# Kernel tuning notes

Measured on AMD Instinct MI355X. Metric: run time of the kernel, lower is better.

The kernel has to match this reference:

```python
import jax, jax.numpy as jnp
import numpy as np

LB_WEIGHT = 0.01  # load_balance_loss_weight


def setup_inputs() -> dict:
    key = jax.random.key(0)
    ks = jax.random.split(key, 5)
    B, S, D, F, E = 2, 2048, 1024, 4096, 8
    scale = 0.02
    return {
        "x": jax.random.normal(ks[0], (B, S, D), dtype=jnp.float32),
        "Wr": jax.random.normal(ks[1], (E, D), dtype=jnp.float32) * scale,
        "W1": jax.random.normal(ks[2], (E, F, D), dtype=jnp.float32) * scale,
        "b1": jnp.zeros((E, F), dtype=jnp.float32),
        "W2": jax.random.normal(ks[3], (E, D, F), dtype=jnp.float32) * scale,
        "b2": jnp.zeros((E, D), dtype=jnp.float32),
        "top_k": 2,
    }


def reference(x, Wr, W1, b1, W2, b2, top_k):
    B, S, D = x.shape
    E = Wr.shape[0]
    x_flat = x.reshape(-1, D)                      # (T, D)

    # Router: softmax over experts, then top-k with renormalized gates.
    router_logits = x_flat @ Wr.T                  # (T, E)
    router_probs = jax.nn.softmax(router_logits, axis=-1)
    topk_p, topk_idx = jax.lax.top_k(router_probs, top_k)   # (T, K)
    topk_p = topk_p / jnp.sum(topk_p, axis=-1, keepdims=True)

    # Combine weights per expert: w[t, e] = sum_k topk_p[t, k] * [idx[t, k] == e]
    one_hot = jax.nn.one_hot(topk_idx, E, dtype=x.dtype)     # (T, K, E)
    combine = jnp.einsum("tk,tke->te", topk_p, one_hot)      # (T, E)

    # Expert FFNs (dense over all experts; masked-out experts get zero weight).
    # FeedForward: Linear(D->F) -> GELU -> Linear(F->D); dropout is identity (eval).
    h = jnp.einsum("td,efd->tef", x_flat, W1) + b1           # (T, E, F)
    h = jax.nn.gelu(h)
    expert_out = jnp.einsum("tef,edf->ted", h, W2) + b2      # (T, E, D)

    out_flat = jnp.einsum("te,ted->td", combine, expert_out) # (T, D)
    output = out_flat.reshape(B, S, D)

    # Load-balance aux loss.
    expert_usage = jnp.mean(router_probs, axis=0)            # (E,)
    aux_loss = LB_WEIGHT * jnp.sum((expert_usage - 1.0 / E) ** 2)
    return output, aux_loss
```

## Files before the change

kernel.cpp:

```cpp
#include <hip/hip_runtime.h>
#include <hip/hip_bf16.h>
#include <stdint.h>

#define D_DIM 1024
#define F_DIM 4096
#define E_NUM 8
#define BM2 256
#define BN2 256
#define BK 64
#define MAXTILES 80
#define MAXT256 40

typedef __attribute__((ext_vector_type(4))) float f32x4;
typedef __attribute__((ext_vector_type(8))) short bf16x8;

#define C_CNT   0
#define C_CUR   8
#define C_OFF   16
#define C_NT    25
#define C_TE    26
#define C_TR    (26+MAXTILES)
#define C_USAGE (26+2*MAXTILES)

__device__ __forceinline__ void gload_lds16(const void* g, void* l) {
  __builtin_amdgcn_global_load_lds((const __attribute__((address_space(1))) void*)g,
                                   (__attribute__((address_space(3))) void*)l, 16, 0, 0);
}

__device__ __forceinline__ float bf2f(unsigned short u) {
  union { unsigned int i; float f; } c; c.i = ((unsigned int)u) << 16; return c.f;
}

__global__ void cvt_k(const float* __restrict__ s, unsigned short* __restrict__ d, int n4) {
  const int stride = gridDim.x * blockDim.x;
  for (int i = blockIdx.x * blockDim.x + threadIdx.x; i < n4; i += stride) {
    float4 v = ((const float4*)s)[i];
    __hip_bfloat16 h0 = __float2bfloat16(v.x);
    __hip_bfloat16 h1 = __float2bfloat16(v.y);
    __hip_bfloat16 h2 = __float2bfloat16(v.z);
    __hip_bfloat16 h3 = __float2bfloat16(v.w);
    ushort4 o;
    o.x = *(unsigned short*)&h0; o.y = *(unsigned short*)&h1;
    o.z = *(unsigned short*)&h2; o.w = *(unsigned short*)&h3;
    ((ushort4*)d)[i] = o;
  }
}

__global__ __launch_bounds__(256) void router_k(
    const float* __restrict__ x, const float* __restrict__ Wr,
    int* __restrict__ t2i, float* __restrict__ t2g,
    float* __restrict__ usage_part, unsigned short* __restrict__ xb, int T) {
  __shared__ float us[4][E_NUM];
  const int wave = threadIdx.x >> 6;
  const int lane = threadIdx.x & 63;
  const int gw = blockIdx.x * 4 + wave;
  const float4* xt = (const float4*)(x + (size_t)gw * D_DIM);
  const float4* wr4 = (const float4*)Wr;
  unsigned short* xrow = xb + (size_t)gw * D_DIM;
  float l[E_NUM] = {0.f,0.f,0.f,0.f,0.f,0.f,0.f,0.f};
#pragma unroll
  for (int it = 0; it < D_DIM / 256; it++) {
    const int i4 = it * 64 + lane;
    const float4 xv = xt[i4];
    __hip_bfloat16 c0 = __float2bfloat16(xv.x), c1 = __float2bfloat16(xv.y);
    __hip_bfloat16 c2 = __float2bfloat16(xv.z), c3 = __float2bfloat16(xv.w);
    ushort4 ov; ov.x = *(unsigned short*)&c0; ov.y = *(unsigned short*)&c1;
    ov.z = *(unsigned short*)&c2; ov.w = *(unsigned short*)&c3;
    ((ushort4*)xrow)[i4] = ov;
#pragma unroll
    for (int e = 0; e < E_NUM; e++) {
      const float4 w = wr4[e * (D_DIM / 4) + i4];
      l[e] += xv.x * w.x + xv.y * w.y + xv.z * w.z + xv.w * w.w;
    }
  }
#pragma unroll
  for (int e = 0; e < E_NUM; e++) {
    float v = l[e];
    v += __shfl_xor(v, 32); v += __shfl_xor(v, 16); v += __shfl_xor(v, 8);
    v += __shfl_xor(v, 4);  v += __shfl_xor(v, 2);  v += __shfl_xor(v, 1);
    l[e] = v;
  }
  float m = l[0];
#pragma unroll
  for (int e = 1; e < E_NUM; e++) m = fmaxf(m, l[e]);
  float p[E_NUM]; float s = 0.f;
#pragma unroll
  for (int e = 0; e < E_NUM; e++) { p[e] = expf(l[e] - m); s += p[e]; }
  const float inv = 1.0f / s;
  float v1 = l[0]; int i1 = 0;
#pragma unroll
  for (int e = 1; e < E_NUM; e++) { if (l[e] > v1) { v1 = l[e]; i1 = e; } }
  float v2 = -3.0e38f; int i2 = 0;
#pragma unroll
  for (int e = 0; e < E_NUM; e++) { if (e != i1 && l[e] > v2) { v2 = l[e]; i2 = e; } }
  const float p1 = expf(v1 - m);
  const float p2 = expf(v2 - m);
  const float gd = 1.0f / (p1 + p2);
  if (lane == 0) {
    t2i[gw * 2] = i1; t2i[gw * 2 + 1] = i2;
    t2g[gw * 2] = p1 * gd; t2g[gw * 2 + 1] = p2 * gd;
#pragma unroll
    for (int e = 0; e < E_NUM; e++) us[wave][e] = p[e] * inv;
  }
  __syncthreads();
  if (threadIdx.x < E_NUM) {
    const int e = threadIdx.x;
    usage_part[blockIdx.x * E_NUM + e] = us[0][e] + us[1][e] + us[2][e] + us[3][e];
  }
}

__global__ __launch_bounds__(256) void reduce_k(
    const float* __restrict__ usage_part, const int* __restrict__ t2i,
    int* __restrict__ ctrl, int nblk, int T2) {
  __shared__ float usum[E_NUM];
  __shared__ int hist[E_NUM];
  if (threadIdx.x < E_NUM) { usum[threadIdx.x] = 0.f; hist[threadIdx.x] = 0; }
  __syncthreads();
  {
    const int e = threadIdx.x & 7;
    const int chunk = threadIdx.x >> 3;
    float s = 0.f;
    for (int i = chunk; i < nblk; i += 32) s += usage_part[i * E_NUM + e];
    atomicAdd(&usum[e], s);
  }
  {
    int h[E_NUM] = {0,0,0,0,0,0,0,0};
    for (int i = threadIdx.x; i < T2; i += 256) h[t2i[i] & 7]++;
#pragma unroll
    for (int e = 0; e < E_NUM; e++) if (h[e]) atomicAdd(&hist[e], h[e]);
  }
  __syncthreads();
  if (threadIdx.x < E_NUM) {
    ctrl[C_CNT + threadIdx.x] = hist[threadIdx.x];
    ((float*)(ctrl + C_USAGE))[threadIdx.x] = usum[threadIdx.x];
  }
}

__global__ void offsets_k(int* __restrict__ ctrl, float* __restrict__ aux_out, int T) {
  if (threadIdx.x == 0) {
    int off = 0, nt = 0;
    for (int e = 0; e < E_NUM; e++) {
      ctrl[C_OFF + e] = off;
      ctrl[C_CUR + e] = off;
      const int c = ctrl[C_CNT + e];
      const int ntile = (c + BM2 - 1) / BM2;
      for (int i = 0; i < ntile; i++) {
        ctrl[C_TE + nt] = e;
        ctrl[C_TR + nt] = off + i * BM2;
        nt++;
      }
      off += c;
    }
    ctrl[C_OFF + E_NUM] = off;
    ctrl[C_NT] = nt;
    const float* usage = (const float*)(ctrl + C_USAGE);
    float loss = 0.f;
    for (int e = 0; e < E_NUM; e++) {
      const float um = usage[e] / (float)T - 1.0f / (float)E_NUM;
      loss += um * um;
    }
    aux_out[0] = 0.01f * loss;
  }
}

__global__ void scatter_k(const int* __restrict__ t2i, int* __restrict__ ctrl,
                          int* __restrict__ rmap, int* __restrict__ slots, int T) {
  const int t = blockIdx.x * blockDim.x + threadIdx.x;
  if (t >= T) return;
#pragma unroll
  for (int k = 0; k < 2; k++) {
    const int e = t2i[t * 2 + k];
    const int slot = atomicAdd(&ctrl[C_CUR + e], 1);
    rmap[slot] = t;
    slots[t * 2 + k] = slot;
  }
}

#define STAGE(K0, AL, BL)                                            \
  {                                                                  \
    _Pragma("unroll")                                                \
    for (int i = 0; i < 4; i++) gload_lds16(a_src[i] + (K0), AL[i]); \
    _Pragma("unroll")                                                \
    for (int i = 0; i < 4; i++) gload_lds16(b_src[i] + (K0), BL[i]); \
  }

#define COMPUTE(AC, BC)                                              \
  {                                                                  \
    _Pragma("unroll")                                                \
    for (int kh = 0; kh < 2; ++kh) {                                 \
      const int co = (((kh * 4 + ckq) ^ swz) << 4);                  \
      bf16x8 af[8], bfv[4];                                          \
      _Pragma("unroll")                                              \
      for (int mi = 0; mi < 8; mi++)                                 \
        af[mi] = *(const bf16x8*)((AC) + (rA + mi * 16) * 128 + co); \
      _Pragma("unroll")                                              \
      for (int ni = 0; ni < 4; ni++)                                 \
        bfv[ni] = *(const bf16x8*)((BC) + (rB + ni * 16) * 128 + co);\
      _Pragma("unroll")                                              \
      for (int mi = 0; mi < 8; mi++)                                 \
        _Pragma("unroll")                                            \
        for (int ni = 0; ni < 4; ni++)                               \
          acc[mi][ni] = __builtin_amdgcn_mfma_f32_16x16x32_bf16(af[mi], bfv[ni], acc[mi][ni], 0, 0, 0); \
    }                                                                \
  }

__global__ __launch_bounds__(512, 2) void gemm1_k(
    const unsigned short* __restrict__ xb, const unsigned short* __restrict__ W1b,
    const float* __restrict__ b1, unsigned short* __restrict__ hb,
    const int* __restrict__ rmap, const int* __restrict__ ctrl, int T2) {
  extern __shared__ char smem[];
  const int lin = blockIdx.x;
  const int lin2 = (lin & 7) * 80 + (lin >> 3);
  const int tile = lin2 >> 4;
  const int fbase = (lin2 & 15) * BN2;

  const int nt = ctrl[C_NT];
  if (tile >= nt) return;
  const int e = ctrl[C_TE + tile];
  const int rowbase = ctrl[C_TR + tile];
  const int row_end = ctrl[C_OFF + e + 1];

  const int tid = threadIdx.x;
  const int lane = tid & 63;
  const int wave = tid >> 6;

  const unsigned short* a_src[4];
  const unsigned short* b_src[4];
  char *aL0[4], *bL0[4], *aL1[4], *bL1[4];
#pragma unroll
  for (int i = 0; i < 4; i++) {
    const int c = tid + 512 * i;
    const int r = c >> 3, cc = c & 7;
    const int sc = cc ^ (r & 7);
    int pos = rowbase + r; pos = pos < T2 ? pos : T2 - 1;
    a_src[i] = xb + (size_t)rmap[pos] * D_DIM + sc * 8;
    b_src[i] = W1b + ((size_t)e * F_DIM + (size_t)(fbase + r)) * D_DIM + sc * 8;
    const int dst = wave * 1024 + i * 8192;
    aL0[i] = smem + dst;          aL1[i] = smem + 32768 + dst;
    bL0[i] = smem + 65536 + dst;  bL1[i] = smem + 98304 + dst;
  }
  const char* As0 = smem;          const char* As1 = smem + 32768;
  const char* Bs0 = smem + 65536;  const char* Bs1 = smem + 98304;

  f32x4 acc[8][4] = {};
  const int wm = wave >> 2, wn = wave & 3;
  const int rA = wm * 128 + (lane & 15);
  const int rB = wn * 64 + (lane & 15);
  const int swz = lane & 7;
  const int ckq = lane >> 4;

  STAGE(0, aL0, bL0);
  const int NK = D_DIM / BK;
  for (int kt = 0; kt < NK; kt += 2) {
    STAGE((kt + 1) * BK, aL1, bL1);
    asm volatile("s_waitcnt vmcnt(8)" ::: "memory");
    __builtin_amdgcn_s_barrier();
    __builtin_amdgcn_sched_barrier(0);
    COMPUTE(As0, Bs0);
    __builtin_amdgcn_sched_barrier(0);
    __builtin_amdgcn_s_barrier();
    if (kt + 2 < NK) {
      STAGE((kt + 2) * BK, aL0, bL0);
      asm volatile("s_waitcnt vmcnt(8)" ::: "memory");
    } else {
      asm volatile("s_waitcnt vmcnt(0)" ::: "memory");
    }
    __builtin_amdgcn_s_barrier();
    __builtin_amdgcn_sched_barrier(0);
    COMPUTE(As1, Bs1);
    __builtin_amdgcn_sched_barrier(0);
    __builtin_amdgcn_s_barrier();
  }

  const int r_rem = row_end - rowbase;
  const float* b1e = b1 + (size_t)e * F_DIM;
  float bias[4];
#pragma unroll
  for (int ni = 0; ni < 4; ni++)
    bias[ni] = b1e[fbase + wn * 64 + ni * 16 + (lane & 15)];
#pragma unroll
  for (int mi = 0; mi < 8; mi++) {
#pragma unroll
    for (int q = 0; q < 4; q++) {
      const int rr = wm * 128 + mi * 16 + (lane >> 4) * 4 + q;
      if (rr < r_rem) {
        unsigned short* hrow = hb + (size_t)(rowbase + rr) * F_DIM;
#pragma unroll
        for (int ni = 0; ni < 4; ni++) {
          const int col = fbase + wn * 64 + ni * 16 + (lane & 15);
          const float v = acc[mi][ni][q] + bias[ni];
          const float u2 = 1.5957691216057308f * (v + 0.044715f * v * v * v);
          const float gg = v / (1.0f + __expf(-u2));
          __hip_bfloat16 hv = __float2bfloat16(gg);
          hrow[col] = *(unsigned short*)&hv;
        }
      }
    }
  }
}

__global__ __launch_bounds__(512, 2) void gemm2_k(
    const unsigned short* __restrict__ hb, const unsigned short* __restrict__ W2b,
    unsigned short* __restrict__ y2, const int* __restrict__ ctrl, int T2) {
  extern __shared__ char smem[];
  const int lin = blockIdx.x;
  const int lin2 = (lin & 7) * 80 + (lin >> 3);
  const int tile = lin2 >> 4;
  const int rest = lin2 & 15;
  const int z = rest >> 2;
  const int dbase = (rest & 3) * BN2;

  const int nt = ctrl[C_NT];
  if (tile >= nt) return;
  const int e = ctrl[C_TE + tile];
  const int rowbase = ctrl[C_TR + tile];
  const int row_end = ctrl[C_OFF + e + 1];
  const int kt0 = z * (F_DIM / BK / 4);

  const int tid = threadIdx.x;
  const int lane = tid & 63;
  const int wave = tid >> 6;

  const unsigned short* a_src[4];
  const unsigned short* b_src[4];
  char *aL0[4], *bL0[4], *aL1[4], *bL1[4];
#pragma unroll
  for (int i = 0; i < 4; i++) {
    const int c = tid + 512 * i;
    const int r = c >> 3, cc = c & 7;
    const int sc = cc ^ (r & 7);
    int pos = rowbase + r; pos = pos < T2 ? pos : T2 - 1;
    a_src[i] = hb + (size_t)pos * F_DIM + sc * 8;
    b_src[i] = W2b + ((size_t)e * D_DIM + (size_t)(dbase + r)) * F_DIM + sc * 8;
    const int dst = wave * 1024 + i * 8192;
    aL0[i] = smem + dst;          aL1[i] = smem + 32768 + dst;
    bL0[i] = smem + 65536 + dst;  bL1[i] = smem + 98304 + dst;
  }
  const char* As0 = smem;          const char* As1 = smem + 32768;
  const char* Bs0 = smem + 65536;  const char* Bs1 = smem + 98304;

  f32x4 acc[8][4] = {};
  const int wm = wave >> 2, wn = wave & 3;
  const int rA = wm * 128 + (lane & 15);
  const int rB = wn * 64 + (lane & 15);
  const int swz = lane & 7;
  const int ckq = lane >> 4;

  const int NKH = F_DIM / BK / 4;
  STAGE(kt0 * BK, aL0, bL0);
  for (int kt = kt0; kt < kt0 + NKH; kt += 2) {
    STAGE((kt + 1) * BK, aL1, bL1);
    asm volatile("s_waitcnt vmcnt(8)" ::: "memory");
    __builtin_amdgcn_s_barrier();
    __builtin_amdgcn_sched_barrier(0);
    COMPUTE(As0, Bs0);
    __builtin_amdgcn_sched_barrier(0);
    __builtin_amdgcn_s_barrier();
    if (kt + 2 < kt0 + NKH) {
      STAGE((kt + 2) * BK, aL0, bL0);
      asm volatile("s_waitcnt vmcnt(8)" ::: "memory");
    } else {
      asm volatile("s_waitcnt vmcnt(0)" ::: "memory");
    }
    __builtin_amdgcn_s_barrier();
    __builtin_amdgcn_sched_barrier(0);
    COMPUTE(As1, Bs1);
    __builtin_amdgcn_sched_barrier(0);
    __builtin_amdgcn_s_barrier();
  }

  const int r_rem = row_end - rowbase;
  unsigned short* yz = y2 + (size_t)z * T2 * D_DIM;
#pragma unroll
  for (int mi = 0; mi < 8; mi++) {
#pragma unroll
    for (int q = 0; q < 4; q++) {
      const int rr = wm * 128 + mi * 16 + (lane >> 4) * 4 + q;
      if (rr < r_rem) {
        unsigned short* yrow = yz + (size_t)(rowbase + rr) * D_DIM;
#pragma unroll
        for (int ni = 0; ni < 4; ni++) {
          const int col = dbase + wn * 64 + ni * 16 + (lane & 15);
          __hip_bfloat16 hv = __float2bfloat16(acc[mi][ni][q]);
          yrow[col] = *(unsigned short*)&hv;
        }
      }
    }
  }
}

__global__ __launch_bounds__(256) void combine_k(
    const unsigned short* __restrict__ y2, const float* __restrict__ b2,
    const int* __restrict__ t2i, const float* __restrict__ t2g,
    const int* __restrict__ slots, float* __restrict__ out, int T2) {
  const int t = blockIdx.x;
  const int c4 = threadIdx.x;
  const int s0 = slots[t * 2], s1 = slots[t * 2 + 1];
  const int e0 = t2i[t * 2], e1 = t2i[t * 2 + 1];
  const float g0 = t2g[t * 2], g1 = t2g[t * 2 + 1];
  const size_t sl = (size_t)T2 * D_DIM;
  float sum0[4] = {0.f,0.f,0.f,0.f}, sum1[4] = {0.f,0.f,0.f,0.f};
#pragma unroll
  for (int zz = 0; zz < 4; zz++) {
    ushort4 a = ((const ushort4*)(y2 + zz * sl + (size_t)s0 * D_DIM))[c4];
    ushort4 b = ((const ushort4*)(y2 + zz * sl + (size_t)s1 * D_DIM))[c4];
    sum0[0] += bf2f(a.x); sum0[1] += bf2f(a.y); sum0[2] += bf2f(a.z); sum0[3] += bf2f(a.w);
    sum1[0] += bf2f(b.x); sum1[1] += bf2f(b.y); sum1[2] += bf2f(b.z); sum1[3] += bf2f(b.w);
  }
  float4 bb0 = ((const float4*)(b2 + (size_t)e0 * D_DIM))[c4];
  float4 bb1 = ((const float4*)(b2 + (size_t)e1 * D_DIM))[c4];
  float4 o;
  o.x = g0 * (sum0[0] + bb0.x) + g1 * (sum1[0] + bb1.x);
  o.y = g0 * (sum0[1] + bb0.y) + g1 * (sum1[1] + bb1.y);
  o.z = g0 * (sum0[2] + bb0.z) + g1 * (sum1[2] + bb1.z);
  o.w = g0 * (sum0[3] + bb0.w) + g1 * (sum1[3] + bb1.w);
  ((float4*)(out + (size_t)t * D_DIM))[c4] = o;
}

extern "C" void kernel_launch(void* const* d_in, const int* in_sizes, int n_in,
                              void* d_out, int out_size, void* d_ws, size_t ws_size,
                              hipStream_t stream) {
  const float* x  = (const float*)d_in[0];
  const float* Wr = (const float*)d_in[1];
  const float* W1 = (const float*)d_in[2];
  const float* b1 = (const float*)d_in[3];
  const float* W2 = (const float*)d_in[4];
  const float* b2 = (const float*)d_in[5];
  float* out = (float*)d_out;

  const int T = in_sizes[0] / D_DIM;
  const int T2 = T * 2;
  const int nblk = T / 4;

  char* ws = (char*)d_ws;
  size_t o = 0;
  unsigned short* xb  = (unsigned short*)(ws + o); o += (size_t)T * D_DIM * 2;
  unsigned short* W1b = (unsigned short*)(ws + o); o += (size_t)E_NUM * F_DIM * D_DIM * 2;
  unsigned short* W2b = (unsigned short*)(ws + o); o += (size_t)E_NUM * D_DIM * F_DIM * 2;
  unsigned short* hb  = (unsigned short*)(ws + o); o += (size_t)T2 * F_DIM * 2;
  int*   ctrl  = (int*)(ws + o);   o += 4096;
  int*   t2i   = (int*)(ws + o);   o += (size_t)T2 * 4;
  float* t2g   = (float*)(ws + o); o += (size_t)T2 * 4;
  int*   rmap  = (int*)(ws + o);   o += (size_t)T2 * 4;
  int*   slots = (int*)(ws + o);   o += (size_t)T2 * 4;
  float* usage_part = (float*)(ws + o); o += (size_t)nblk * E_NUM * 4;
  unsigned short* y2 = W1b;

  hipFuncSetAttribute((const void*)gemm1_k, hipFuncAttributeMaxDynamicSharedMemorySize, 131072);
  hipFuncSetAttribute((const void*)gemm2_k, hipFuncAttributeMaxDynamicSharedMemorySize, 131072);

  hipMemsetAsync(ctrl, 0, 4096, stream);

  cvt_k<<<1024, 256, 0, stream>>>(W1, W1b, E_NUM * F_DIM * D_DIM / 4);
  cvt_k<<<1024, 256, 0, stream>>>(W2, W2b, E_NUM * D_DIM * F_DIM / 4);

  router_k<<<nblk, 256, 0, stream>>>(x, Wr, t2i, t2g, usage_part, xb, T);
  reduce_k<<<1, 256, 0, stream>>>(usage_part, t2i, ctrl, nblk, T2);
  offsets_k<<<1, 64, 0, stream>>>(ctrl, out + (size_t)(out_size - 1), T);
  scatter_k<<<(T + 255) / 256, 256, 0, stream>>>(t2i, ctrl, rmap, slots, T);

  gemm1_k<<<MAXT256 * 16, 512, 131072, stream>>>(xb, W1b, b1, hb, rmap, ctrl, T2);
  gemm2_k<<<MAXT256 * 16, 512, 131072, stream>>>(hb, W2b, y2, ctrl, T2);
  combine_k<<<T, 256, 0, stream>>>(y2, b2, t2i, t2g, slots, out, T2);
}
```

Before: 380.1 us.

## Replace double-buffered BK64 GEMM loop with four-stage BK32 pipeline and column-major LDS

Both expert GEMM kernels now run a 4-deep ring of 32 KB LDS stages, each holding a K=32 slice, in place of the old double-buffered K=64 loop. The LDS layout changes to chunk-major (k-chunk by row) with no XOR swizzle, and MFMA issue is wrapped in s_setprio. Deeper prefetch is meant to hide global latency better. In exchange, launch bounds drop to one block per CU, which lowers occupancy and doubles the number of barriers per unit of K.

```diff
diff --git a/kernel.cpp b/kernel.cpp
--- a/kernel.cpp
+++ b/kernel.cpp
@@ -7,7 +7,6 @@
 #define E_NUM 8
 #define BM2 256
 #define BN2 256
-#define BK 64
 #define MAXTILES 80
 #define MAXT256 40
 
@@ -176,35 +175,53 @@
   }
 }
 
-#define STAGE(K0, AL, BL)                                            \
+
+#define STAGE_S(S)                                                   \
   {                                                                  \
+    char* rb_ = smem + ((S) & 3) * 32768;                            \
     _Pragma("unroll")                                                \
-    for (int i = 0; i < 4; i++) gload_lds16(a_src[i] + (K0), AL[i]); \
+    for (int j = 0; j < 4; j++)                                      \
+      gload_lds16(src[j] + (size_t)(S) * 32, rb_ + dq[j]);           \
+  }
+
+#define PHASE(S)                                                     \
+  {                                                                  \
+    __builtin_amdgcn_s_barrier();         \
+    __builtin_amdgcn_sched_barrier(0);                               \
+    const char* rb_ = smem + ((S) & 3) * 32768;                      \
+    bf16x8 af[8], bfv[4];                                            \
     _Pragma("unroll")                                                \
-    for (int i = 0; i < 4; i++) gload_lds16(b_src[i] + (K0), BL[i]); \
-  }
-
-#define COMPUTE(AC, BC)                                              \
-  {                                                                  \
+    for (int mi = 0; mi < 8; mi++)                                   \
+      af[mi] = *(const bf16x8*)(rb_ + abase + mi * 256);             \
     _Pragma("unroll")                                                \
-    for (int kh = 0; kh < 2; ++kh) {                                 \
-      const int co = (((kh * 4 + ckq) ^ swz) << 4);                  \
-      bf16x8 af[8], bfv[4];                                          \
-      _Pragma("unroll")                                              \
-      for (int mi = 0; mi < 8; mi++)                                 \
-        af[mi] = *(const bf16x8*)((AC) + (rA + mi * 16) * 128 + co); \
+    for (int ni = 0; ni < 4; ni++)                                   \
+      bfv[ni] = *(const bf16x8*)(rb_ + bbase + ni * 256);            \
+    asm volatile("s_waitcnt lgkmcnt(0)" ::: "memory");               \
+    __builtin_amdgcn_sched_barrier(0);                               \
+    __builtin_amdgcn_s_setprio(1);                                   \
+    _Pragma("unroll")                                                \
+    for (int mi = 0; mi < 8; mi++)                                   \
       _Pragma("unroll")                                              \
       for (int ni = 0; ni < 4; ni++)                                 \
-        bfv[ni] = *(const bf16x8*)((BC) + (rB + ni * 16) * 128 + co);\
-      _Pragma("unroll")                                              \
-      for (int mi = 0; mi < 8; mi++)                                 \
-        _Pragma("unroll")                                            \
-        for (int ni = 0; ni < 4; ni++)                               \
-          acc[mi][ni] = __builtin_amdgcn_mfma_f32_16x16x32_bf16(af[mi], bfv[ni], acc[mi][ni], 0, 0, 0); \
-    }                                                                \
-  }
-
-__global__ __launch_bounds__(512, 2) void gemm1_k(
+        acc[mi][ni] = __builtin_amdgcn_mfma_f32_16x16x32_bf16(af[mi], bfv[ni], acc[mi][ni], 0, 0, 0); \
+    __builtin_amdgcn_s_setprio(0);                                   \
+    __builtin_amdgcn_sched_barrier(0);                               \
+    __builtin_amdgcn_s_barrier();           \
+  }
+
+#define KLOOP(NS)                                                    \
+  asm volatile("s_waitcnt vmcnt(0)" ::: "memory");  \
+  STAGE_S(0); STAGE_S(1); STAGE_S(2);                                \
+  for (int s = 0; s < (NS) - 3; ++s) {                               \
+    STAGE_S(s + 3);                                                  \
+    asm volatile("s_waitcnt vmcnt(12)" ::: "memory");                \
+    PHASE(s);                                                        \
+  }                                                                  \
+  asm volatile("s_waitcnt vmcnt(8)" ::: "memory");  PHASE((NS) - 3); \
+  asm volatile("s_waitcnt vmcnt(4)" ::: "memory");  PHASE((NS) - 2); \
+  asm volatile("s_waitcnt vmcnt(0)" ::: "memory");  PHASE((NS) - 1);
+
+__global__ __launch_bounds__(512, 1) void gemm1_k(
     const unsigned short* __restrict__ xb, const unsigned short* __restrict__ W1b,
     const float* __restrict__ b1, unsigned short* __restrict__ hb,
     const int* __restrict__ rmap, const int* __restrict__ ctrl, int T2) {
@@ -223,54 +240,29 @@
   const int tid = threadIdx.x;
   const int lane = tid & 63;
   const int wave = tid >> 6;
-
-  const unsigned short* a_src[4];
-  const unsigned short* b_src[4];
-  char *aL0[4], *bL0[4], *aL1[4], *bL1[4];
-#pragma unroll
-  for (int i = 0; i < 4; i++) {
-    const int c = tid + 512 * i;
-    const int r = c >> 3, cc = c & 7;
-    const int sc = cc ^ (r & 7);
-    int pos = rowbase + r; pos = pos < T2 ? pos : T2 - 1;
-    a_src[i] = xb + (size_t)rmap[pos] * D_DIM + sc * 8;
-    b_src[i] = W1b + ((size_t)e * F_DIM + (size_t)(fbase + r)) * D_DIM + sc * 8;
-    const int dst = wave * 1024 + i * 8192;
-    aL0[i] = smem + dst;          aL1[i] = smem + 32768 + dst;
-    bL0[i] = smem + 65536 + dst;  bL1[i] = smem + 98304 + dst;
-  }
-  const char* As0 = smem;          const char* As1 = smem + 32768;
-  const char* Bs0 = smem + 65536;  const char* Bs1 = smem + 98304;
+  const int wm = wave >> 2, wn = wave & 3;
+
+  const unsigned short* src[4]; int dq[4];
+#pragma unroll
+  for (int j = 0; j < 4; j++) {
+    const int q = j * 512 + tid;
+    dq[j] = q * 16;
+    if (q < 1024) {
+      const int c = q >> 8, row = q & 255;
+      int pos = rowbase + row; pos = pos < T2 ? pos : T2 - 1;
+      src[j] = xb + (size_t)rmap[pos] * D_DIM + c * 8;
+    } else {
+      const int qq = q - 1024;
+      const int c = qq >> 8, col = qq & 255;
+      src[j] = W1b + ((size_t)e * F_DIM + (size_t)(fbase + col)) * D_DIM + c * 8;
+    }
+  }
 
   f32x4 acc[8][4] = {};
-  const int wm = wave >> 2, wn = wave & 3;
-  const int rA = wm * 128 + (lane & 15);
-  const int rB = wn * 64 + (lane & 15);
-  const int swz = lane & 7;
-  const int ckq = lane >> 4;
-
-  STAGE(0, aL0, bL0);
-  const int NK = D_DIM / BK;
-  for (int kt = 0; kt < NK; kt += 2) {
-    STAGE((kt + 1) * BK, aL1, bL1);
-    asm volatile("s_waitcnt vmcnt(8)" ::: "memory");
-    __builtin_amdgcn_s_barrier();
-    __builtin_amdgcn_sched_barrier(0);
-    COMPUTE(As0, Bs0);
-    __builtin_amdgcn_sched_barrier(0);
-    __builtin_amdgcn_s_barrier();
-    if (kt + 2 < NK) {
-      STAGE((kt + 2) * BK, aL0, bL0);
-      asm volatile("s_waitcnt vmcnt(8)" ::: "memory");
-    } else {
-      asm volatile("s_waitcnt vmcnt(0)" ::: "memory");
-    }
-    __builtin_amdgcn_s_barrier();
-    __builtin_amdgcn_sched_barrier(0);
-    COMPUTE(As1, Bs1);
-    __builtin_amdgcn_sched_barrier(0);
-    __builtin_amdgcn_s_barrier();
-  }
+  const int abase = (lane >> 4) * 4096 + wm * 2048 + (lane & 15) * 16;
+  const int bbase = 16384 + (lane >> 4) * 4096 + wn * 1024 + (lane & 15) * 16;
+
+  KLOOP(D_DIM / 32);
 
   const int r_rem = row_end - rowbase;
   const float* b1e = b1 + (size_t)e * F_DIM;
@@ -299,7 +291,7 @@
   }
 }
 
-__global__ __launch_bounds__(512, 2) void gemm2_k(
+__global__ __launch_bounds__(512, 1) void gemm2_k(
     const unsigned short* __restrict__ hb, const unsigned short* __restrict__ W2b,
     unsigned short* __restrict__ y2, const int* __restrict__ ctrl, int T2) {
   extern __shared__ char smem[];
@@ -315,59 +307,34 @@
   const int e = ctrl[C_TE + tile];
   const int rowbase = ctrl[C_TR + tile];
   const int row_end = ctrl[C_OFF + e + 1];
-  const int kt0 = z * (F_DIM / BK / 4);
+  const int kbase = z * (F_DIM / 4);
 
   const int tid = threadIdx.x;
   const int lane = tid & 63;
   const int wave = tid >> 6;
-
-  const unsigned short* a_src[4];
-  const unsigned short* b_src[4];
-  char *aL0[4], *bL0[4], *aL1[4], *bL1[4];
-#pragma unroll
-  for (int i = 0; i < 4; i++) {
-    const int c = tid + 512 * i;
-    const int r = c >> 3, cc = c & 7;
-    const int sc = cc ^ (r & 7);
-    int pos = rowbase + r; pos = pos < T2 ? pos : T2 - 1;
-    a_src[i] = hb + (size_t)pos * F_DIM + sc * 8;
-    b_src[i] = W2b + ((size_t)e * D_DIM + (size_t)(dbase + r)) * F_DIM + sc * 8;
-    const int dst = wave * 1024 + i * 8192;
-    aL0[i] = smem + dst;          aL1[i] = smem + 32768 + dst;
-    bL0[i] = smem + 65536 + dst;  bL1[i] = smem + 98304 + dst;
-  }
-  const char* As0 = smem;          const char* As1 = smem + 32768;
-  const char* Bs0 = smem + 65536;  const char* Bs1 = smem + 98304;
+  const int wm = wave >> 2, wn = wave & 3;
+
+  const unsigned short* src[4]; int dq[4];
+#pragma unroll
+  for (int j = 0; j < 4; j++) {
+    const int q = j * 512 + tid;
+    dq[j] = q * 16;
+    if (q < 1024) {
+      const int c = q >> 8, row = q & 255;
+      int pos = rowbase + row; pos = pos < T2 ? pos : T2 - 1;
+      src[j] = hb + (size_t)pos * F_DIM + kbase + c * 8;
+    } else {
+      const int qq = q - 1024;
+      const int c = qq >> 8, col = qq & 255;
+      src[j] = W2b + ((size_t)e * D_DIM + (size_t)(dbase + col)) * F_DIM + kbase + c * 8;
+    }
+  }
 
   f32x4 acc[8][4] = {};
-  const int wm = wave >> 2, wn = wave & 3;
-  const int rA = wm * 128 + (lane & 15);
-  const int rB = wn * 64 + (lane & 15);
-  const int swz = lane & 7;
-  const int ckq = lane >> 4;
-
-  const int NKH = F_DIM / BK / 4;
-  STAGE(kt0 * BK, aL0, bL0);
-  for (int kt = kt0; kt < kt0 + NKH; kt += 2) {
-    STAGE((kt + 1) * BK, aL1, bL1);
-    asm volatile("s_waitcnt vmcnt(8)" ::: "memory");
-    __builtin_amdgcn_s_barrier();
-    __builtin_amdgcn_sched_barrier(0);
-    COMPUTE(As0, Bs0);
-    __builtin_amdgcn_sched_barrier(0);
-    __builtin_amdgcn_s_barrier();
-    if (kt + 2 < kt0 + NKH) {
-      STAGE((kt + 2) * BK, aL0, bL0);
-      asm volatile("s_waitcnt vmcnt(8)" ::: "memory");
-    } else {
-      asm volatile("s_waitcnt vmcnt(0)" ::: "memory");
-    }
-    __builtin_amdgcn_s_barrier();
-    __builtin_amdgcn_sched_barrier(0);
-    COMPUTE(As1, Bs1);
-    __builtin_amdgcn_sched_barrier(0);
-    __builtin_amdgcn_s_barrier();
-  }
+  const int abase = (lane >> 4) * 4096 + wm * 2048 + (lane & 15) * 16;
+  const int bbase = 16384 + (lane >> 4) * 4096 + wn * 1024 + (lane & 15) * 16;
+
+  KLOOP(F_DIM / 4 / 32);
 
   const int r_rem = row_end - rowbase;
   unsigned short* yz = y2 + (size_t)z * T2 * D_DIM;
```

After: 505.9 us. 33.1% more time.
